# Kernel tuning notes

Hardware: AMD Instinct MI355X
Metric: run time of the kernel (lower is better)

The kernel has to match this reference:

```python
import jax, jax.numpy as jnp
import numpy as np

HEADS = 4

def _axial_attn(xs, wqkv, wproj, bproj, heads=HEADS):
    # xs: [B', C, L]; wqkv: [3C, C]; wproj: [C, C]; bproj: [C]
    Bp, C, L = xs.shape
    hd = C // heads
    scale = hd ** -0.5
    qkv = jnp.einsum('oc,bcl->bol', wqkv, xs)  # [B', 3C, L]
    q, k, v = jnp.split(qkv, 3, axis=1)
    q = q.reshape(Bp, heads, hd, L)
    k = k.reshape(Bp, heads, hd, L)
    v = v.reshape(Bp, heads, hd, L)
    attn = jax.nn.softmax(jnp.einsum('bhdi,bhdj->bhij', q, k) * scale, axis=-1)
    out = jnp.einsum('bhij,bhdj->bhdi', attn, v).reshape(Bp, C, L)
    return jnp.einsum('oc,bcl->bol', wproj, out) + bproj[None, :, None]

def setup_inputs() -> dict:
    key = jax.random.key(0)
    ks = jax.random.split(key, 7)
    B, C, H, W = 8, 128, 128, 128
    return {
        'x': jax.random.normal(ks[0], (B, C, H, W), dtype=jnp.float32),
        'wqkv_h': jax.random.normal(ks[1], (3 * C, C), dtype=jnp.float32) * 0.05,
        'wproj_h': jax.random.normal(ks[2], (C, C), dtype=jnp.float32) * 0.05,
        'bproj_h': jax.random.normal(ks[3], (C,), dtype=jnp.float32) * 0.05,
        'wqkv_w': jax.random.normal(ks[4], (3 * C, C), dtype=jnp.float32) * 0.05,
        'wproj_w': jax.random.normal(ks[5], (C, C), dtype=jnp.float32) * 0.05,
        'bproj_w': jax.random.normal(ks[6], (C,), dtype=jnp.float32) * 0.05,
    }

def reference(x, wqkv_h, wproj_h, bproj_h, wqkv_w, wproj_w, bproj_w):
    B, C, H, W = x.shape
    # height pass: rows become batch, attend along W
    xh = x.transpose(0, 2, 1, 3).reshape(B * H, C, W)
    xh = _axial_attn(xh, wqkv_h, wproj_h, bproj_h)
    xh = xh.reshape(B, H, C, W).transpose(0, 2, 1, 3)
    # width pass: cols become batch, attend along H
    xw = x.transpose(0, 3, 1, 2).reshape(B * W, C, H)
    xw = _axial_attn(xw, wqkv_w, wproj_w, bproj_w)
    xw = xw.reshape(B, W, C, H).transpose(0, 2, 3, 1)
    return (xh + xw) / 2
```

## Files before the change

kernel.cpp:

```cpp
#include <hip/hip_runtime.h>
#include <hip/hip_bf16.h>
#include <stdint.h>

typedef __attribute__((ext_vector_type(8))) short short8v;
typedef __attribute__((ext_vector_type(4))) float f32x4;
typedef unsigned short u16;
typedef unsigned int u32;

__device__ __align__(16) u16 g_xh [8u * 128u * 128u * 128u];
__device__ __align__(16) u16 g_xTw[8u * 128u * 128u * 128u];
__device__ __align__(16) u16 g_W1 [8u * 128u * 128u * 128u];
__device__ __align__(16) u16 g_W2 [8u * 128u * 128u * 128u];
__device__ __align__(16) u16 g_wqkvP[2u * 49152u];
__device__ __align__(16) u16 g_wpP [2u * 16384u];

#define XST_OFF 0
#define QT_OFF  32768
#define KT_OFF  43008
#define VH_OFF  53248
#define SMEM_BYTES 61952

__device__ __forceinline__ u16 f2bf(float f) {
    u32 b = __float_as_uint(f);
    b += 0x7FFFu + ((b >> 16) & 1u);
    return (u16)(b >> 16);
}
__device__ __forceinline__ u32 pk2(float a, float b) {
    __hip_bfloat162 h = __float22bfloat162_rn(make_float2(a, b));
    union { __hip_bfloat162 h; u32 u; } cv; cv.h = h; return cv.u;
}
__device__ __forceinline__ float bf2f(u16 u) {
    return __uint_as_float(((u32)u) << 16);
}

__global__ __launch_bounds__(512)
void prep_weights(const float* __restrict__ wqkv_h, const float* __restrict__ wproj_h,
                  const float* __restrict__ wqkv_w, const float* __restrict__ wproj_w)
{
    const float QSC = 0.17677669529663687f * 1.4426950408889634f;
    int id = blockIdx.x * 512 + threadIdx.x;
    if (id < 12288) {
        int p = id / 6144, i2 = id % 6144;
        int h = i2 / 1536, i3 = i2 % 1536;
        int t = i3 / 256,  i4 = i3 % 256;
        int kk = i4 / 64,  lane = i4 % 64;
        int cc = lane & 15, qq = lane >> 4;
        int r96 = t * 16 + cc;
        int g = r96 >> 5, rl = r96 & 31;
        const float* src = (p == 0 ? wqkv_h : wqkv_w) + (g * 128 + h * 32 + rl) * 128 + kk * 32 + qq * 8;
        float4 a = *(const float4*)src;
        float4 c = *(const float4*)(src + 4);
        float s = (g == 0) ? QSC : 1.0f;
        *(uint4*)(g_wqkvP + (size_t)id * 8) =
            make_uint4(pk2(a.x * s, a.y * s), pk2(a.z * s, a.w * s),
                       pk2(c.x * s, c.y * s), pk2(c.z * s, c.w * s));
    } else {
        int id2 = id - 12288;
        int p = id2 / 2048, i2 = id2 % 2048;
        int h = i2 / 512,  i3 = i2 % 512;
        int t = i3 / 64,   lane = i3 % 64;
        int cc = lane & 15, qq = lane >> 4;
        int o = t * 16 + cc;
        const float* src = (p == 0 ? wproj_h : wproj_w) + o * 128 + h * 32 + qq * 8;
        float4 a = *(const float4*)src;
        float4 c = *(const float4*)(src + 4);
        *(uint4*)(g_wpP + (size_t)id2 * 8) =
            make_uint4(pk2(a.x * 0.5f, a.y * 0.5f), pk2(a.z * 0.5f, a.w * 0.5f),
                       pk2(c.x * 0.5f, c.y * 0.5f), pk2(c.z * 0.5f, c.w * 0.5f));
    }
}

__global__ __launch_bounds__(256)
void transpose_x(const float* __restrict__ x)
{
    __shared__ char tsm[32768];
    const int b = blockIdx.x >> 6;
    const int hp = blockIdx.x & 63;
    const int tid = threadIdx.x;
    for (int hh = 0; hh < 2; ++hh) {
        const int h = hp * 2 + hh;
        #pragma unroll
        for (int it = 0; it < 16; ++it) {
            int task = it * 256 + tid;
            int w = task & 127, c4 = task >> 7;
            const float* p = x + (size_t)b * 2097152 + (c4 * 4) * 16384 + h * 128 + w;
            u32 u0 = pk2(p[0], p[16384]);
            u32 u1 = pk2(p[2 * 16384], p[3 * 16384]);
            int off = w * 256 + ((((c4 >> 1) << 4) ^ ((w & 7) << 4)) | ((c4 & 1) << 3));
            *(uint2*)(tsm + off) = make_uint2(u0, u1);
        }
        __syncthreads();
        #pragma unroll
        for (int it = 0; it < 8; ++it) {
            int i = it * 256 + tid;
            *(uint4*)(g_xh + (size_t)(b * 128 + h) * 16384 + i * 8) = *(const uint4*)(tsm + i * 16);
        }
        #pragma unroll
        for (int it = 0; it < 8; ++it) {
            int i = it * 256 + tid;
            int w = i >> 4, c8 = i & 15;
            uint4 v = *(const uint4*)(tsm + w * 256 + ((c8 << 4) ^ ((w & 7) << 4)));
            size_t ds = ((size_t)(b * 128 + w) * 128 + h) * 128 + (((c8 << 4) ^ ((h & 7) << 4)) >> 1);
            *(uint4*)(g_xTw + ds) = v;
        }
        __syncthreads();
    }
}

__global__ __launch_bounds__(512, 4)
void attn_kernel(const float* __restrict__ bias_h, const float* __restrict__ bias_w)
{
    extern __shared__ char smem[];
    const int t    = threadIdx.x;
    const int lane = t & 63;
    const int wv   = t >> 6;
    const int cc   = lane & 15;
    const int qq   = lane >> 4;
    const int pass = blockIdx.x >> 10;
    const int b    = (blockIdx.x >> 7) & 7;
    const int row  = blockIdx.x & 127;
    const f32x4 zf4 = (f32x4){0.f, 0.f, 0.f, 0.f};

    {
        const u16* slab = (pass ? g_xTw : g_xh) + (size_t)(b * 128 + row) * 16384;
        #pragma unroll
        for (int it = 0; it < 4; ++it) {
            int idx = t + 512 * it;
            *(uint4*)(smem + XST_OFF + idx * 16) = *(const uint4*)(slab + idx * 8);
        }
    }

    const float* bias = pass ? bias_w : bias_h;

    f32x4 yacc[8];
    #pragma unroll
    for (int i = 0; i < 8; ++i) yacc[i] = zf4;

    __syncthreads();

    const int og = wv & 1;
    const int lg = wv >> 1;

    for (int h = 0; h < 4; ++h) {
        const u16* wb  = g_wqkvP + (size_t)(pass * 4 + h) * 12288;
        const u16* wpb = g_wpP   + (size_t)(pass * 4 + h) * 4096;

        {
            f32x4 acc[3][2];
            #pragma unroll
            for (int ot = 0; ot < 3; ++ot)
                #pragma unroll
                for (int lt = 0; lt < 2; ++lt) acc[ot][lt] = zf4;
            __builtin_amdgcn_s_setprio(1);
            #pragma unroll
            for (int kk = 0; kk < 4; ++kk) {
                short8v A[3], Bf[2];
                #pragma unroll
                for (int ot = 0; ot < 3; ++ot)
                    A[ot] = *(const short8v*)(wb + (((og * 3 + ot) * 4 + kk) * 64 + lane) * 8);
                #pragma unroll
                for (int lt = 0; lt < 2; ++lt) {
                    int l = lg * 32 + lt * 16 + cc;
                    Bf[lt] = *(const short8v*)(smem + XST_OFF + l * 256 + (((kk * 64 + qq * 16)) ^ ((l & 7) << 4)));
                }
                #pragma unroll
                for (int ot = 0; ot < 3; ++ot)
                    #pragma unroll
                    for (int lt = 0; lt < 2; ++lt)
                        acc[ot][lt] = __builtin_amdgcn_mfma_f32_16x16x32_bf16(A[ot], Bf[lt], acc[ot][lt], 0, 0, 0);
            }
            __builtin_amdgcn_s_setprio(0);
            #pragma unroll
            for (int ot = 0; ot < 3; ++ot) {
                int got = og * 3 + ot;
                #pragma unroll
                for (int lt = 0; lt < 2; ++lt) {
                    int l0 = (lg * 2 + lt) * 16 + cc;
                    f32x4 v = acc[ot][lt];
                    if (got < 2) {
                        *(uint2*)(smem + QT_OFF + l0 * 80 + (got * 16 + 4 * qq) * 2) =
                            make_uint2(pk2(v[0], v[1]), pk2(v[2], v[3]));
                    } else if (got < 4) {
                        *(uint2*)(smem + KT_OFF + l0 * 80 + ((got - 2) * 16 + 4 * qq) * 2) =
                            make_uint2(pk2(v[0], v[1]), pk2(v[2], v[3]));
                    } else {
                        int d0 = (got - 4) * 16 + 4 * qq;
                        #pragma unroll
                        for (int r = 0; r < 4; ++r)
                            *(u16*)(smem + VH_OFF + (d0 + r) * 272 + l0 * 2) = f2bf(v[r]);
                    }
                }
            }
        }
        __syncthreads();

        f32x4 sacc[8];
        {
            short8v aq = *(const short8v*)(smem + QT_OFF + (wv * 16 + cc) * 80 + qq * 16);
            __builtin_amdgcn_s_setprio(1);
            #pragma unroll
            for (int jt = 0; jt < 8; ++jt) {
                short8v bk = *(const short8v*)(smem + KT_OFF + (jt * 16 + cc) * 80 + qq * 16);
                sacc[jt] = __builtin_amdgcn_mfma_f32_16x16x32_bf16(bk, aq, zf4, 0, 0, 0);
            }
            __builtin_amdgcn_s_setprio(0);
        }
        float mx = -3.4e38f;
        #pragma unroll
        for (int jt = 0; jt < 8; ++jt)
            #pragma unroll
            for (int r = 0; r < 4; ++r) mx = fmaxf(mx, sacc[jt][r]);
        mx = fmaxf(mx, __shfl_xor(mx, 16));
        mx = fmaxf(mx, __shfl_xor(mx, 32));
        float sm = 0.f;
        #pragma unroll
        for (int jt = 0; jt < 8; ++jt)
            #pragma unroll
            for (int r = 0; r < 4; ++r) {
                float p = exp2f(sacc[jt][r] - mx);
                sacc[jt][r] = p;
                sm += p;
            }
        sm += __shfl_xor(sm, 16);
        sm += __shfl_xor(sm, 32);
        float rden = 1.0f / sm;
        u32 u[8][2];
        #pragma unroll
        for (int jt = 0; jt < 8; ++jt) {
            u[jt][0] = pk2(sacc[jt][0], sacc[jt][1]);
            u[jt][1] = pk2(sacc[jt][2], sacc[jt][3]);
        }

        f32x4 oacc[2] = {zf4, zf4};
        const int base = cc + ((qq & 1) << 5);
        const bool hiT = (qq >> 1) != 0;
        __builtin_amdgcn_s_setprio(1);
        #pragma unroll
        for (int kt = 0; kt < 4; ++kt) {
            int a0 = __shfl((int)u[2 * kt][0], base),      a1 = __shfl((int)u[2 * kt][1], base);
            int a2 = __shfl((int)u[2 * kt][0], base + 16), a3 = __shfl((int)u[2 * kt][1], base + 16);
            int b0 = __shfl((int)u[2 * kt + 1][0], base),      b1 = __shfl((int)u[2 * kt + 1][1], base);
            int b2 = __shfl((int)u[2 * kt + 1][0], base + 16), b3 = __shfl((int)u[2 * kt + 1][1], base + 16);
            union { uint4 u4; short8v s8; } pf;
            pf.u4 = make_uint4((u32)(hiT ? b0 : a0), (u32)(hiT ? b1 : a1),
                               (u32)(hiT ? b2 : a2), (u32)(hiT ? b3 : a3));
            #pragma unroll
            for (int dt = 0; dt < 2; ++dt) {
                short8v vf = *(const short8v*)(smem + VH_OFF + (dt * 16 + cc) * 272 + kt * 64 + qq * 16);
                oacc[dt] = __builtin_amdgcn_mfma_f32_16x16x32_bf16(vf, pf.s8, oacc[dt], 0, 0, 0);
            }
        }
        __builtin_amdgcn_s_setprio(0);

        if (h < 3) __syncthreads();

        union { uint4 u4; short8v s8; } of;
        {
            u32 o00 = pk2(oacc[0][0] * rden, oacc[0][1] * rden);
            u32 o01 = pk2(oacc[0][2] * rden, oacc[0][3] * rden);
            u32 o10 = pk2(oacc[1][0] * rden, oacc[1][1] * rden);
            u32 o11 = pk2(oacc[1][2] * rden, oacc[1][3] * rden);
            u32 a0 = (u32)__shfl((int)o00, base),      a1 = (u32)__shfl((int)o01, base);
            u32 c0 = (u32)__shfl((int)o10, base),      c1 = (u32)__shfl((int)o11, base);
            u32 b0 = (u32)__shfl((int)o00, base + 16), b1 = (u32)__shfl((int)o01, base + 16);
            u32 d0 = (u32)__shfl((int)o10, base + 16), d1 = (u32)__shfl((int)o11, base + 16);
            of.u4 = make_uint4(hiT ? c0 : a0, hiT ? c1 : a1, hiT ? d0 : b0, hiT ? d1 : b1);
        }
        {
            __builtin_amdgcn_s_setprio(1);
            #pragma unroll
            for (int ot = 0; ot < 8; ++ot) {
                short8v aw = *(const short8v*)(wpb + ((size_t)(ot * 64 + lane)) * 8);
                yacc[ot] = __builtin_amdgcn_mfma_f32_16x16x32_bf16(aw, of.s8, yacc[ot], 0, 0, 0);
            }
            __builtin_amdgcn_s_setprio(0);
        }
    }

    u16* dst = pass ? g_W2 : g_W1;
    const int l = wv * 16 + cc;
    #pragma unroll
    for (int ot = 0; ot < 8; ++ot) {
        float4 bb = *(const float4*)(bias + ot * 16 + 4 * qq);
        u32 p01 = pk2(yacc[ot][0] + bb.x * 0.5f, yacc[ot][1] + bb.y * 0.5f);
        u32 p23 = pk2(yacc[ot][2] + bb.z * 0.5f, yacc[ot][3] + bb.w * 0.5f);
        int o0 = ot * 16 + 4 * qq;
        size_t idx = ((size_t)(b * 128 + o0) * 128 + row) * 128 + l;
        dst[idx]         = (u16)p01;
        dst[idx + 16384] = (u16)(p01 >> 16);
        dst[idx + 32768] = (u16)p23;
        dst[idx + 49152] = (u16)(p23 >> 16);
    }
}

__global__ __launch_bounds__(256)
void merge_w(float* __restrict__ out)
{
    __shared__ char msm[128 * 264];
    const int b = blockIdx.x >> 7;
    const int o = blockIdx.x & 127;
    const int tid = threadIdx.x;
    const u16* slab = g_W2 + (size_t)(b * 128 + o) * 16384;
    #pragma unroll
    for (int it = 0; it < 8; ++it) {
        int i = it * 256 + tid;
        int w = i >> 4, h8 = i & 15;
        *(uint4*)(msm + w * 264 + h8 * 16) = *(const uint4*)(slab + w * 128 + h8 * 8);
    }
    __syncthreads();
    const u16* w1p = g_W1 + (size_t)(b * 128 + o) * 16384;
    float* op = out + (size_t)(b * 128 + o) * 16384;
    #pragma unroll
    for (int it = 0; it < 8; ++it) {
        int i = it * 256 + tid;
        int h = i >> 4, w8 = i & 15;
        uint4 w1 = *(const uint4*)(w1p + h * 128 + w8 * 8);
        float f[8];
        #pragma unroll
        for (int k = 0; k < 8; ++k)
            f[k] = bf2f(*(const u16*)(msm + (w8 * 8 + k) * 264 + h * 2));
        float* dp = op + h * 128 + w8 * 8;
        float4 v0, v1;
        v0.x = f[0] + bf2f((u16)(w1.x & 0xFFFF));
        v0.y = f[1] + bf2f((u16)(w1.x >> 16));
        v0.z = f[2] + bf2f((u16)(w1.y & 0xFFFF));
        v0.w = f[3] + bf2f((u16)(w1.y >> 16));
        v1.x = f[4] + bf2f((u16)(w1.z & 0xFFFF));
        v1.y = f[5] + bf2f((u16)(w1.z >> 16));
        v1.z = f[6] + bf2f((u16)(w1.w & 0xFFFF));
        v1.w = f[7] + bf2f((u16)(w1.w >> 16));
        *(float4*)dp = v0;
        *(float4*)(dp + 4) = v1;
    }
}

extern "C" void kernel_launch(void* const* d_in, const int* in_sizes, int n_in,
                              void* d_out, int out_size, void* d_ws, size_t ws_size,
                              hipStream_t stream)
{
    const float* x       = (const float*)d_in[0];
    const float* wqkv_h  = (const float*)d_in[1];
    const float* wproj_h = (const float*)d_in[2];
    const float* bproj_h = (const float*)d_in[3];
    const float* wqkv_w  = (const float*)d_in[4];
    const float* wproj_w = (const float*)d_in[5];
    const float* bproj_w = (const float*)d_in[6];
    float* out = (float*)d_out;

    (void)hipFuncSetAttribute((const void*)attn_kernel,
                              hipFuncAttributeMaxDynamicSharedMemorySize, SMEM_BYTES);

    prep_weights<<<dim3(32), dim3(512), 0, stream>>>(wqkv_h, wproj_h, wqkv_w, wproj_w);
    transpose_x<<<dim3(512), dim3(256), 0, stream>>>(x);
    attn_kernel<<<dim3(2048), dim3(512), SMEM_BYTES, stream>>>(bproj_h, bproj_w);
    merge_w<<<dim3(1024), dim3(256), 0, stream>>>(out);
}
```

Measured before the change: 182.8 us.

## Cache X fragments in registers and double-buffer QKV to drop a barrier

```diff
diff --git a/kernel.cpp b/kernel.cpp
--- a/kernel.cpp
+++ b/kernel.cpp
@@ -14,10 +14,6 @@
 __device__ __align__(16) u16 g_wqkvP[2u * 49152u];
 __device__ __align__(16) u16 g_wpP [2u * 16384u];
 
-#define XST_OFF 0
-#define QT_OFF  32768
-#define KT_OFF  43008
-#define VH_OFF  53248
 #define SMEM_BYTES 61952
 
 __device__ __forceinline__ u16 f2bf(float f) {
@@ -126,7 +122,7 @@
         #pragma unroll
         for (int it = 0; it < 4; ++it) {
             int idx = t + 512 * it;
-            *(uint4*)(smem + XST_OFF + idx * 16) = *(const uint4*)(slab + idx * 8);
+            *(uint4*)(smem + idx * 16) = *(const uint4*)(slab + idx * 8);
         }
     }
 
@@ -140,10 +136,23 @@
 
     const int og = wv & 1;
     const int lg = wv >> 1;
+
+    short8v xf[2][4];
+    #pragma unroll
+    for (int lt = 0; lt < 2; ++lt) {
+        int l = lg * 32 + lt * 16 + cc;
+        #pragma unroll
+        for (int kk = 0; kk < 4; ++kk)
+            xf[lt][kk] = *(const short8v*)(smem + l * 256 + ((kk * 64 + qq * 16) ^ ((l & 7) << 4)));
+    }
 
     for (int h = 0; h < 4; ++h) {
         const u16* wb  = g_wqkvP + (size_t)(pass * 4 + h) * 12288;
         const u16* wpb = g_wpP   + (size_t)(pass * 4 + h) * 4096;
+        const int bb   = (h & 1) ? 0 : 32768;
+        char* QT = smem + bb;
+        char* KT = smem + bb + 10240;
+        char* VH = smem + bb + 20480;
 
         {
             f32x4 acc[3][2];
@@ -154,20 +163,15 @@
             __builtin_amdgcn_s_setprio(1);
             #pragma unroll
             for (int kk = 0; kk < 4; ++kk) {
-                short8v A[3], Bf[2];
+                short8v A[3];
                 #pragma unroll
                 for (int ot = 0; ot < 3; ++ot)
                     A[ot] = *(const short8v*)(wb + (((og * 3 + ot) * 4 + kk) * 64 + lane) * 8);
                 #pragma unroll
-                for (int lt = 0; lt < 2; ++lt) {
-                    int l = lg * 32 + lt * 16 + cc;
-                    Bf[lt] = *(const short8v*)(smem + XST_OFF + l * 256 + (((kk * 64 + qq * 16)) ^ ((l & 7) << 4)));
-                }
-                #pragma unroll
                 for (int ot = 0; ot < 3; ++ot)
                     #pragma unroll
                     for (int lt = 0; lt < 2; ++lt)
-                        acc[ot][lt] = __builtin_amdgcn_mfma_f32_16x16x32_bf16(A[ot], Bf[lt], acc[ot][lt], 0, 0, 0);
+                        acc[ot][lt] = __builtin_amdgcn_mfma_f32_16x16x32_bf16(A[ot], xf[lt][kk], acc[ot][lt], 0, 0, 0);
             }
             __builtin_amdgcn_s_setprio(0);
             #pragma unroll
@@ -178,16 +182,16 @@
                     int l0 = (lg * 2 + lt) * 16 + cc;
                     f32x4 v = acc[ot][lt];
                     if (got < 2) {
-                        *(uint2*)(smem + QT_OFF + l0 * 80 + (got * 16 + 4 * qq) * 2) =
+                        *(uint2*)(QT + l0 * 80 + (got * 16 + 4 * qq) * 2) =
                             make_uint2(pk2(v[0], v[1]), pk2(v[2], v[3]));
                     } else if (got < 4) {
-                        *(uint2*)(smem + KT_OFF + l0 * 80 + ((got - 2) * 16 + 4 * qq) * 2) =
+                        *(uint2*)(KT + l0 * 80 + ((got - 2) * 16 + 4 * qq) * 2) =
                             make_uint2(pk2(v[0], v[1]), pk2(v[2], v[3]));
                     } else {
                         int d0 = (got - 4) * 16 + 4 * qq;
                         #pragma unroll
                         for (int r = 0; r < 4; ++r)
-                            *(u16*)(smem + VH_OFF + (d0 + r) * 272 + l0 * 2) = f2bf(v[r]);
+                            *(u16*)(VH + (d0 + r) * 272 + l0 * 2) = f2bf(v[r]);
                     }
                 }
             }
@@ -196,11 +200,11 @@
 
         f32x4 sacc[8];
         {
-            short8v aq = *(const short8v*)(smem + QT_OFF + (wv * 16 + cc) * 80 + qq * 16);
+            short8v aq = *(const short8v*)(QT + (wv * 16 + cc) * 80 + qq * 16);
             __builtin_amdgcn_s_setprio(1);
             #pragma unroll
             for (int jt = 0; jt < 8; ++jt) {
-                short8v bk = *(const short8v*)(smem + KT_OFF + (jt * 16 + cc) * 80 + qq * 16);
+                short8v bk = *(const short8v*)(KT + (jt * 16 + cc) * 80 + qq * 16);
                 sacc[jt] = __builtin_amdgcn_mfma_f32_16x16x32_bf16(bk, aq, zf4, 0, 0, 0);
             }
             __builtin_amdgcn_s_setprio(0);
@@ -246,13 +250,11 @@
                                (u32)(hiT ? b2 : a2), (u32)(hiT ? b3 : a3));
             #pragma unroll
             for (int dt = 0; dt < 2; ++dt) {
-                short8v vf = *(const short8v*)(smem + VH_OFF + (dt * 16 + cc) * 272 + kt * 64 + qq * 16);
+                short8v vf = *(const short8v*)(VH + (dt * 16 + cc) * 272 + kt * 64 + qq * 16);
                 oacc[dt] = __builtin_amdgcn_mfma_f32_16x16x32_bf16(vf, pf.s8, oacc[dt], 0, 0, 0);
             }
         }
         __builtin_amdgcn_s_setprio(0);
-
-        if (h < 3) __syncthreads();
 
         union { uint4 u4; short8v s8; } of;
         {
```

Result: slower. 202.8 us (+10.9%).
